# Kernel tuning notes

Measured on AMD Instinct MI355X. Metric: run time of the kernel, lower is better.

The kernel has to match this reference:

```python
import jax, jax.numpy as jnp
import numpy as np

B, C, H, W = 256, 3, 224, 224
NP, PS = 14, 16          # patches per row, patch size
D, NH, NB = 192, 4, 3    # hidden_d, num_heads (Block default), n_blocks
OUT = 1000
T = NP * NP + 1          # tokens incl. class token


def _lin(x, w, b):
    # torch nn.Linear: y = x @ W^T + b, W is [out, in]
    return x @ w.T + b


def setup_inputs() -> dict:
    key = jax.random.key(0)
    ks = jax.random.split(key, 22)
    n = lambda k, shp: jax.random.normal(k, shp, dtype=jnp.float32) * 0.02
    return {
        "x": jax.random.normal(ks[0], (B, C, H, W), dtype=jnp.float32),
        "lm_w": n(ks[1], (D, C * PS * PS)), "lm_b": n(ks[2], (D,)),
        "cls_tok": jax.random.uniform(ks[3], (1, D), dtype=jnp.float32),  # torch.rand
        "pos_emb": n(ks[4], (T, D)),
        # per-block params stacked on leading dim NB
        "q_w": n(ks[5], (NB, D, D)), "q_b": n(ks[6], (NB, D)),
        "k_w": n(ks[7], (NB, D, D)), "k_b": n(ks[8], (NB, D)),
        "v_w": n(ks[9], (NB, D, D)), "v_b": n(ks[10], (NB, D)),
        "in_w": n(ks[11], (NB, 3 * D, D)), "in_b": n(ks[12], (NB, 3 * D)),
        "out_w": n(ks[13], (NB, D, D)), "out_b": n(ks[14], (NB, D)),
        "up_w": n(ks[15], (NB, 4 * D, D)), "up_b": n(ks[16], (NB, 4 * D)),
        "down_w": n(ks[17], (NB, D, 4 * D)), "down_b": n(ks[18], (NB, D)),
        "head_w": n(ks[19], (OUT, D)), "head_b": n(ks[20], (OUT,)),
    }


def reference(x, lm_w, lm_b, cls_tok, pos_emb, q_w, q_b, k_w, k_b, v_w, v_b,
              in_w, in_b, out_w, out_b, up_w, up_b, down_w, down_b, head_w, head_b):
    N = x.shape[0]
    # vectorized patchify: [N,C,H,W] -> [N, NP*NP, C*PS*PS] (flatten order C,ps,ps matches torch)
    patches = x.reshape(N, C, NP, PS, NP, PS).transpose(0, 2, 4, 1, 3, 5).reshape(N, NP * NP, C * PS * PS)
    tok = _lin(patches, lm_w, lm_b)
    tok = jnp.concatenate([jnp.broadcast_to(cls_tok[None], (N, 1, D)), tok], axis=1) + pos_emb[None]
    dh = D // NH
    scale = 1.0 / np.sqrt(dh).astype(np.float32)
    for i in range(NB):
        # Block's own q/k/v projections
        q = _lin(tok, q_w[i], q_b[i])
        k = _lin(tok, k_w[i], k_b[i])
        v = _lin(tok, v_w[i], v_b[i])
        # nn.MultiheadAttention internal in_proj (applied on top of q/k/v)
        wq, wk, wv = jnp.split(in_w[i], 3, axis=0)
        bq, bk, bv = jnp.split(in_b[i], 3, axis=0)
        qh = _lin(q, wq, bq).reshape(N, T, NH, dh).transpose(0, 2, 1, 3)
        kh = _lin(k, wk, bk).reshape(N, T, NH, dh).transpose(0, 2, 1, 3)
        vh = _lin(v, wv, bv).reshape(N, T, NH, dh).transpose(0, 2, 1, 3)
        scores = jnp.einsum('bhqd,bhkd->bhqk', qh, kh) * scale
        attn = jax.nn.softmax(scores, axis=-1)
        o = jnp.einsum('bhqk,bhkd->bhqd', attn, vh).transpose(0, 2, 1, 3).reshape(N, T, D)
        o = _lin(o, out_w[i], out_b[i])  # MHA out_proj
        tok = tok + o                     # residual around attention only
        tok = _lin(jax.nn.relu(_lin(tok, up_w[i], up_b[i])), down_w[i], down_b[i])  # MLP, no residual
    cls = tok[:, 0, :]
    return _lin(cls, head_w, head_b)
```

## Files before the change

### kernel.cpp

```cpp
#include <hip/hip_runtime.h>

typedef unsigned short u16;
typedef __bf16 bf16x8 __attribute__((ext_vector_type(8)));
typedef float  f32x4  __attribute__((ext_vector_type(4)));
typedef u16    u16x8  __attribute__((ext_vector_type(8)));

#define BATCH 256
#define TT    197
#define TP    256
#define DD    192
#define DHP   64
#define MTOK  (BATCH*TT)
#define MPAT  (BATCH*196)

constexpr size_t BIG_E  = 1024ull*256*256;
constexpr size_t TOK_E  = (size_t)MTOK*DD;
constexpr size_t QKV_E  = 1024ull*TP*DHP;

__device__ __forceinline__ float b2f(u16 h){ union{unsigned u; float f;} x; x.u=(unsigned)h<<16; return x.f; }
__device__ __forceinline__ u16 f2b(float f){ union{float f; unsigned u;} x{f}; unsigned r = x.u + 0x7fffu + ((x.u>>16)&1u); return (u16)(r>>16); }
__device__ __forceinline__ bf16x8 as_bf(u16x8 v){ return __builtin_bit_cast(bf16x8, v); }

__device__ __forceinline__ void gload_lds16(const void* g, void* l) {
  __builtin_amdgcn_global_load_lds((__attribute__((address_space(1))) void*)(size_t)g,
                                   (__attribute__((address_space(3))) void*)l, 16, 0, 0);
}

enum { M_F32=0, M_BF16=1, M_QKV=2, M_PATCH=4 };

template<int MODE, bool RELU, bool RES, bool BIAS>
__global__ __launch_bounds__(256)
void gemm4w(const u16* __restrict__ A, const u16* __restrict__ W,
            const float* __restrict__ bias, const u16* __restrict__ res,
            void* __restrict__ Cout, const float* __restrict__ aux,
            int K, int lda, int ldc, int Nreal,
            long bA, long bW, long bC)
{
  __shared__ __align__(16) u16 As[2][256*32];
  __shared__ __align__(16) u16 Ws[2][64*32];
  const int tid  = threadIdx.x;
  const int wv   = tid >> 6;
  const int lane = tid & 63;

  const int nN  = gridDim.x, nM = gridDim.y;
  const int nwg = nN * nM;
  const int fid = blockIdx.x + nN * blockIdx.y;
  const int xcd = fid & 7, loc = fid >> 3;
  const int q8  = nwg >> 3, r8 = nwg & 7;
  const int tile = (xcd < r8 ? xcd * (q8 + 1) : r8 * (q8 + 1) + (xcd - r8) * q8) + loc;
  const int m0 = (tile / nN) * 256;
  const int n0 = (tile % nN) * 64;

  const int bz = blockIdx.z;
  const u16* Ab = A + (size_t)bz * (size_t)bA;
  const u16* Wb = W + (size_t)bz * (size_t)bW;

  const int lrow = lane & 15, quad = lane >> 4;
  const int srow = lane >> 2, sseg = lane & 3;
  const int wsw  = (srow >> 1) & 3;
  const int rsw  = (lrow >> 1) & 3;

  f32x4 acc[4][4];
  #pragma unroll
  for (int i=0;i<4;i++)
    #pragma unroll
    for (int j=0;j<4;j++) { f32x4 z = {0.f,0.f,0.f,0.f}; acc[i][j] = z; }

  auto stage = [&](int bufi, int k0) {
    #pragma unroll
    for (int i=0;i<4;i++) {
      const u16* ga = Ab + (size_t)(m0 + i*64 + wv*16 + srow)*lda + (k0 + (sseg^wsw)*8);
      gload_lds16(ga, &As[bufi][(i*64 + wv*16)*32]);
    }
    const u16* gw = Wb + (size_t)(n0 + wv*16 + srow)*K + (k0 + (sseg^wsw)*8);
    gload_lds16(gw, &Ws[bufi][(wv*16)*32]);
  };

  const int nt = K >> 5;
  stage(0, 0);
  int cur = 0;
  for (int t = 0; t < nt; ++t) {
    if (t + 1 < nt) {
      stage(cur ^ 1, (t + 1) << 5);
      asm volatile("s_waitcnt vmcnt(5)" ::: "memory");
    } else {
      asm volatile("s_waitcnt vmcnt(0)" ::: "memory");
    }
    asm volatile("s_barrier" ::: "memory");

    bf16x8 af[4], wf[4];
    #pragma unroll
    for (int i=0;i<4;i++) {
      af[i] = *(const bf16x8*)&As[cur][(wv*64 + i*16 + lrow)*32 + (quad^rsw)*8];
      wf[i] = *(const bf16x8*)&Ws[cur][(i*16 + lrow)*32 + (quad^rsw)*8];
    }
    #pragma unroll
    for (int mi=0;mi<4;mi++)
      #pragma unroll
      for (int ni=0;ni<4;ni++)
        acc[mi][ni] = __builtin_amdgcn_mfma_f32_16x16x32_bf16(af[mi], wf[ni], acc[mi][ni], 0,0,0);

    asm volatile("s_waitcnt lgkmcnt(0)" ::: "memory");
    asm volatile("s_barrier" ::: "memory");
    cur ^= 1;
  }

  #pragma unroll
  for (int mi=0;mi<4;mi++) {
    #pragma unroll
    for (int ni=0;ni<4;ni++) {
      #pragma unroll
      for (int r=0;r<4;r++) {
        int row = m0 + wv*64 + mi*16 + quad*4 + r;
        int col = n0 + ni*16 + lrow;
        float v = acc[mi][ni][r];
        if constexpr (MODE == M_F32) {
          if (col < Nreal) {
            if constexpr (BIAS) v += bias[col];
            ((float*)Cout)[(size_t)row*ldc + col] = v;
          }
        } else if constexpr (MODE == M_BF16) {
          if constexpr (BIAS) v += bias[col];
          if constexpr (RES)  v += b2f(res[(size_t)row*ldc + col]);
          if constexpr (RELU) v = v > 0.f ? v : 0.f;
          ((u16*)Cout)[(size_t)bz*(size_t)bC + (size_t)row*ldc + col] = f2b(v);
        } else if constexpr (MODE == M_QKV) {
          v += bias[col];
          int sel = col / 192, rem = col % 192;
          int h = rem / 48, d = rem % 48;
          int b = row / 197, t = row % 197;
          ((u16*)Cout)[(size_t)sel*QKV_E + ((size_t)(b*4 + h)*TP + t)*DHP + d] = f2b(v);
        } else if constexpr (MODE == M_PATCH) {
          int b = row / 196, p = row % 196;
          v += bias[col] + aux[(size_t)(1 + p)*DD + col];
          ((u16*)Cout)[((size_t)(b*197) + 1 + p)*DD + col] = f2b(v);
        }
      }
    }
  }
}

#define KSTR 72
#define VSTR 216
#define PSTR 72
#define TKR  208

__global__ __launch_bounds__(256,1)
void flash_k(const u16* __restrict__ Qg, const u16* __restrict__ Kg,
             const u16* __restrict__ Vg, u16* __restrict__ Og)
{
  __shared__ __align__(16) u16 Ks[TKR*KSTR];
  __shared__ __align__(16) u16 Vs[49*VSTR];
  __shared__ __align__(16) u16 Ps[4*16*PSTR];
  const int bh = blockIdx.x;
  const int b = bh >> 2, h = bh & 3;
  const int tid = threadIdx.x, wv = tid >> 6, lane = tid & 63;
  const int lrow = lane & 15, quad = lane >> 4;
  const size_t base = (size_t)bh * TP * DHP;
  const float scale = 0.14433756729740643f;

  bf16x8 qf[4][2];
  #pragma unroll
  for (int rg=0; rg<4; rg++)
    #pragma unroll
    for (int ka=0; ka<2; ka++)
      qf[rg][ka] = as_bf(*(const u16x8*)(Qg + base + (size_t)(wv*64+rg*16+lrow)*DHP + ka*32 + quad*8));

  for (int it=0; it<5; it++) {
    int slot = it*256 + tid;
    if (slot < 1248) {
      int t = slot/6, sg = slot - t*6;
      u16x8 v = *(const u16x8*)(Kg + base + (size_t)t*DHP + sg*8);
      *(u16x8*)&Ks[t*KSTR + sg*8] = v;
    }
  }
  {
    u16x8 z = {0,0,0,0,0,0,0,0};
    for (int it=0; it<2; it++) {
      int slot = it*256 + tid;
      if (slot < 416) { int t = slot>>1, sg = 6 + (slot&1);
        *(u16x8*)&Ks[t*KSTR + sg*8] = z; }
    }
  }
  for (int it=0; it<5; it++) {
    int slot = it*256 + tid;
    if (slot < 1248) {
      int sg = slot/208, t = slot - sg*208;
      u16x8 v = *(const u16x8*)(Vg + base + (size_t)t*DHP + sg*8);
      #pragma unroll
      for (int j=0;j<8;j++) Vs[(sg*8+j)*VSTR + t] = v[j];
    }
  }
  __syncthreads();

  f32x4 o[4][3];
  float m_i[4][4], l_i[4][4];
  #pragma unroll
  for (int rg=0;rg<4;rg++) {
    #pragma unroll
    for (int dg=0;dg<3;dg++) { f32x4 z = {0.f,0.f,0.f,0.f}; o[rg][dg] = z; }
    #pragma unroll
    for (int r=0;r<4;r++) { m_i[rg][r] = -1e30f; l_i[rg][r] = 0.f; }
  }
  u16* Pw = &Ps[wv*16*PSTR];

  #pragma unroll
  for (int c=0; c<4; c++) {
    const int NC = (c<3) ? 4 : 1;
    f32x4 s[4][4];
    #pragma unroll
    for (int rg=0;rg<4;rg++)
      #pragma unroll
      for (int cg=0;cg<4;cg++) if (cg < NC) { f32x4 z = {0.f,0.f,0.f,0.f}; s[rg][cg] = z; }

    #pragma unroll
    for (int cg=0;cg<4;cg++) if (cg < NC) {
      #pragma unroll
      for (int ka=0; ka<2; ka++) {
        bf16x8 kf = as_bf(*(const u16x8*)&Ks[(c*64+cg*16+lrow)*KSTR + ka*32 + quad*8]);
        #pragma unroll
        for (int rg=0;rg<4;rg++)
          s[rg][cg] = __builtin_amdgcn_mfma_f32_16x16x32_bf16(qf[rg][ka], kf, s[rg][cg], 0,0,0);
      }
    }

    #pragma unroll
    for (int rg=0;rg<4;rg++) {
      if (c == 3) {
        #pragma unroll
        for (int r=0;r<4;r++) s[rg][0][r] = (lrow >= 5) ? -1e30f : s[rg][0][r];
      }
      float mnew[4], al[4];
      #pragma unroll
      for (int r=0;r<4;r++) {
        float mc = s[rg][0][r];
        #pragma unroll
        for (int cg=1;cg<4;cg++) if (cg < NC) mc = fmaxf(mc, s[rg][cg][r]);
        #pragma unroll
        for (int sh=1; sh<16; sh<<=1) mc = fmaxf(mc, __shfl_xor(mc, sh, 64));
        float mo = m_i[rg][r];
        float mn = fmaxf(mo, mc);
        mnew[r] = mn;
        al[r] = __expf((mo - mn)*scale);
      }
      #pragma unroll
      for (int r=0;r<4;r++) {
        float acc = 0.f;
        #pragma unroll
        for (int cg=0;cg<4;cg++) if (cg < NC) {
          float p = __expf((s[rg][cg][r] - mnew[r])*scale);
          s[rg][cg][r] = p;
          acc += p;
        }
        #pragma unroll
        for (int sh=1; sh<16; sh<<=1) acc += __shfl_xor(acc, sh, 64);
        l_i[rg][r] = l_i[rg][r]*al[r] + acc;
        m_i[rg][r] = mnew[r];
      }
      #pragma unroll
      for (int dg=0;dg<3;dg++)
        #pragma unroll
        for (int r=0;r<4;r++) o[rg][dg][r] *= al[r];

      #pragma unroll
      for (int cg=0;cg<4;cg++) if (cg < NC) {
        #pragma unroll
        for (int r=0;r<4;r++)
          Pw[(quad*4+r)*PSTR + cg*16 + lrow] = f2b(s[rg][cg][r]);
      }
      if (c == 3) {
        #pragma unroll
        for (int r=0;r<4;r++) Pw[(quad*4+r)*PSTR + 16 + lrow] = 0;
      }
      __builtin_amdgcn_s_waitcnt(0xC07F);

      const int NK = (c<3) ? 2 : 1;
      #pragma unroll
      for (int ka=0; ka<2; ka++) if (ka < NK) {
        bf16x8 pf = as_bf(*(const u16x8*)&Pw[lrow*PSTR + ka*32 + quad*8]);
        #pragma unroll
        for (int dg=0;dg<3;dg++) {
          bf16x8 vf = as_bf(*(const u16x8*)&Vs[(dg*16+lrow)*VSTR + c*64 + ka*32 + quad*8]);
          o[rg][dg] = __builtin_amdgcn_mfma_f32_16x16x32_bf16(pf, vf, o[rg][dg], 0,0,0);
        }
      }
      __builtin_amdgcn_s_waitcnt(0xC07F);
    }
  }

  #pragma unroll
  for (int rg=0;rg<4;rg++) {
    #pragma unroll
    for (int r=0;r<4;r++) {
      int t = wv*64 + rg*16 + quad*4 + r;
      if (t < 197) {
        float inv = 1.0f / l_i[rg][r];
        u16* dst = Og + ((size_t)(b*197) + t)*DD + h*48;
        #pragma unroll
        for (int dg=0;dg<3;dg++) dst[dg*16 + lrow] = f2b(o[rg][dg][r]*inv);
      }
    }
  }
}

__global__ void cvt5_k(const float* __restrict__ a, const float* __restrict__ b,
                       const float* __restrict__ c, const float* __restrict__ d,
                       const float* __restrict__ e,
                       u16* __restrict__ oa, u16* __restrict__ ob, u16* __restrict__ oc,
                       u16* __restrict__ od, u16* __restrict__ oe) {
  int i = blockIdx.x*256 + threadIdx.x;
  if (i < 147456) { oa[i] = f2b(a[i]); return; } i -= 147456;
  if (i < 110592) { ob[i] = f2b(b[i]); return; } i -= 110592;
  if (i < 442368) { oc[i] = f2b(c[i]); return; } i -= 442368;
  if (i < 442368) { od[i] = f2b(d[i]); return; } i -= 442368;
  if (i < 196608) { oe[i] = (i < 192000) ? f2b(e[i]) : (u16)0; }
}

__global__ void im2col_k(const float* __restrict__ x, u16* __restrict__ P) {
  int id = blockIdx.x*256 + threadIdx.x;
  int w8 = id % 28; int r = id / 28;
  int h  = r % 224; r /= 224;
  int c  = r % 3;   int b = r / 3;
  const float* src = x + (((size_t)(b*3 + c)*224 + h)*224 + w8*8);
  float4 a  = *(const float4*)src;
  float4 bb = *(const float4*)(src + 4);
  int pr = h >> 4, i = h & 15, pc = (w8*8) >> 4, j0 = (w8*8) & 15;
  u16* dst = P + ((size_t)(b*196) + pr*14 + pc)*768 + (c*256 + i*16 + j0);
  u16x8 o;
  o[0]=f2b(a.x); o[1]=f2b(a.y); o[2]=f2b(a.z); o[3]=f2b(a.w);
  o[4]=f2b(bb.x); o[5]=f2b(bb.y); o[6]=f2b(bb.z); o[7]=f2b(bb.w);
  *(u16x8*)dst = o;
}

__global__ void cls_k(const float* __restrict__ cls_tok, const float* __restrict__ pos, u16* __restrict__ tok) {
  int b = blockIdx.x, d = threadIdx.x;
  tok[((size_t)b*197)*DD + d] = f2b(cls_tok[d] + pos[d]);
}

__global__ void fusew_k(const float* __restrict__ in_w, const float* __restrict__ q_w,
                        const float* __restrict__ k_w, const float* __restrict__ v_w,
                        u16* __restrict__ weff) {
  int i = blockIdx.x, p = blockIdx.y, n = blockIdx.z;
  int k = threadIdx.x;
  const float* wrow = in_w + ((size_t)i*576 + p*192 + n)*192;
  const float* Bm = (p==0 ? q_w : (p==1 ? k_w : v_w)) + (size_t)i*192*192;
  float acc = 0.f;
  for (int m=0;m<192;m++) acc += wrow[m] * Bm[m*192 + k];
  weff[((size_t)i*576 + p*192 + n)*192 + k] = f2b(acc);
}

__global__ void fuseb_k(const float* __restrict__ in_w, const float* __restrict__ q_b,
                        const float* __restrict__ k_b, const float* __restrict__ v_b,
                        const float* __restrict__ in_b, float* __restrict__ effb) {
  int i = blockIdx.x, n = threadIdx.x;
  int p = n / 192;
  const float* bb = (p==0 ? q_b : (p==1 ? k_b : v_b)) + i*192;
  const float* wrow = in_w + ((size_t)i*576 + n)*192;
  float acc = in_b[i*576 + n];
  for (int m=0;m<192;m++) acc += wrow[m]*bb[m];
  effb[i*576 + n] = acc;
}

extern "C" void kernel_launch(void* const* d_in, const int* in_sizes, int n_in,
                              void* d_out, int out_size, void* d_ws, size_t ws_size,
                              hipStream_t stream) {
  const float* x      = (const float*)d_in[0];
  const float* lm_w   = (const float*)d_in[1];
  const float* lm_b   = (const float*)d_in[2];
  const float* cls_t  = (const float*)d_in[3];
  const float* pos    = (const float*)d_in[4];
  const float* q_w    = (const float*)d_in[5];
  const float* q_b    = (const float*)d_in[6];
  const float* k_w    = (const float*)d_in[7];
  const float* k_b    = (const float*)d_in[8];
  const float* v_w    = (const float*)d_in[9];
  const float* v_b    = (const float*)d_in[10];
  const float* in_w   = (const float*)d_in[11];
  const float* in_b   = (const float*)d_in[12];
  const float* out_w  = (const float*)d_in[13];
  const float* out_b  = (const float*)d_in[14];
  const float* up_w   = (const float*)d_in[15];
  const float* up_b   = (const float*)d_in[16];
  const float* dn_w   = (const float*)d_in[17];
  const float* dn_b   = (const float*)d_in[18];
  const float* head_w = (const float*)d_in[19];
  const float* head_b = (const float*)d_in[20];

  char* ws = (char*)d_ws;
  size_t off = 0;
  auto alloc = [&](size_t elems, size_t esz) {
    void* p = ws + off; off += ((elems*esz + 255)/256)*256; return p;
  };
  u16*  big  = (u16*)alloc(BIG_E, 2);
  u16*  tok  = (u16*)alloc(TOK_E, 2);
  u16*  qq   = (u16*)alloc(QKV_E*3, 2);
  u16*  obuf = (u16*)alloc(TOK_E, 2);
  u16*  lmw  = (u16*)alloc(147456, 2);
  u16*  outw = (u16*)alloc(110592, 2);
  u16*  upw  = (u16*)alloc(442368, 2);
  u16*  dnw  = (u16*)alloc(442368, 2);
  u16*  hdw  = (u16*)alloc(196608, 2);
  u16*  weff = (u16*)alloc(331776, 2);
  float* effb = (float*)alloc(1728, 4);
  (void)ws_size; (void)in_sizes; (void)n_in; (void)out_size;

  u16* kbuf = qq + QKV_E;
  u16* vbuf = qq + 2*QKV_E;

  cvt5_k<<<(1339392+255)/256,256,0,stream>>>(lm_w, out_w, up_w, dn_w, head_w,
                                             lmw, outw, upw, dnw, hdw);
  fusew_k<<<dim3(3,3,192),192,0,stream>>>(in_w, q_w, k_w, v_w, weff);
  fuseb_k<<<3,576,0,stream>>>(in_w, q_b, k_b, v_b, in_b, effb);

  im2col_k<<<18816,256,0,stream>>>(x, big);
  gemm4w<M_PATCH,false,false,true><<<dim3(3,MPAT/256,1),256,0,stream>>>(
      big, lmw, lm_b, nullptr, tok, pos, 768, 768, DD, DD, 0,0,0);
  cls_k<<<BATCH,DD,0,stream>>>(cls_t, pos, tok);

  for (int i=0;i<3;i++) {
    gemm4w<M_QKV,false,false,true><<<dim3(9,MTOK/256,1),256,0,stream>>>(
        tok, weff + (size_t)i*576*192, effb + i*576, nullptr, qq, nullptr,
        192, 192, 0, 576, 0,0,0);
    flash_k<<<1024,256,0,stream>>>(qq, kbuf, vbuf, obuf);
    gemm4w<M_BF16,false,true,true><<<dim3(3,MTOK/256,1),256,0,stream>>>(
        obuf, outw + (size_t)i*36864, out_b + i*192, tok, tok, nullptr,
        192, 192, DD, DD, 0,0,0);
    gemm4w<M_BF16,true,false,true><<<dim3(12,MTOK/256,1),256,0,stream>>>(
        tok, upw + (size_t)i*147456, up_b + i*768, nullptr, big, nullptr,
        192, 192, 768, 768, 0,0,0);
    gemm4w<M_BF16,false,false,true><<<dim3(3,MTOK/256,1),256,0,stream>>>(
        big, dnw + (size_t)i*147456, dn_b + i*192, nullptr, tok, nullptr,
        768, 768, DD, DD, 0,0,0);
  }
  gemm4w<M_F32,false,false,true><<<dim3(16,1,1),256,0,stream>>>(
      tok, hdw, head_b, nullptr, d_out, nullptr,
      192, 197*192, 1000, 1000, 0,0,0);
}
```

Measured before the change: 981.5 us.

## Halve GEMM M-tile, triple-buffer LDS, and software-pipeline flash P·V

The GEMM kernel's M tile shrinks from 256 to 128 rows, giving twice as many workgroups. It moves from double to triple buffering, prefetching two K-steps ahead with a single barrier per iteration instead of two. The flash attention kernel double-buffers the P scratch per wave so the P·V MFMAs for the previous row group overlap the softmax of the current one, with the last P·V drained after the loop. Risks include the single-barrier triple-buffer race safety and more LDS traffic per FLOP from smaller tiles. MTOK=50432 is divisible by 128, so the grid changes stay consistent.

```diff
diff --git a/kernel.cpp b/kernel.cpp
--- a/kernel.cpp
+++ b/kernel.cpp
@@ -36,8 +36,8 @@
             int K, int lda, int ldc, int Nreal,
             long bA, long bW, long bC)
 {
-  __shared__ __align__(16) u16 As[2][256*32];
-  __shared__ __align__(16) u16 Ws[2][64*32];
+  __shared__ __align__(16) u16 As[3][128*32];
+  __shared__ __align__(16) u16 Ws[3][64*32];
   const int tid  = threadIdx.x;
   const int wv   = tid >> 6;
   const int lane = tid & 63;
@@ -48,7 +48,7 @@
   const int xcd = fid & 7, loc = fid >> 3;
   const int q8  = nwg >> 3, r8 = nwg & 7;
   const int tile = (xcd < r8 ? xcd * (q8 + 1) : r8 * (q8 + 1) + (xcd - r8) * q8) + loc;
-  const int m0 = (tile / nN) * 256;
+  const int m0 = (tile / nN) * 128;
   const int n0 = (tile % nN) * 64;
 
   const int bz = blockIdx.z;
@@ -60,15 +60,15 @@
   const int wsw  = (srow >> 1) & 3;
   const int rsw  = (lrow >> 1) & 3;
 
-  f32x4 acc[4][4];
-  #pragma unroll
-  for (int i=0;i<4;i++)
+  f32x4 acc[2][4];
+  #pragma unroll
+  for (int i=0;i<2;i++)
     #pragma unroll
     for (int j=0;j<4;j++) { f32x4 z = {0.f,0.f,0.f,0.f}; acc[i][j] = z; }
 
   auto stage = [&](int bufi, int k0) {
     #pragma unroll
-    for (int i=0;i<4;i++) {
+    for (int i=0;i<2;i++) {
       const u16* ga = Ab + (size_t)(m0 + i*64 + wv*16 + srow)*lda + (k0 + (sseg^wsw)*8);
       gload_lds16(ga, &As[bufi][(i*64 + wv*16)*32]);
     }
@@ -78,40 +78,38 @@
 
   const int nt = K >> 5;
   stage(0, 0);
-  int cur = 0;
+  stage(1, 32);
   for (int t = 0; t < nt; ++t) {
     if (t + 1 < nt) {
-      stage(cur ^ 1, (t + 1) << 5);
-      asm volatile("s_waitcnt vmcnt(5)" ::: "memory");
+      asm volatile("s_waitcnt vmcnt(3)" ::: "memory");
     } else {
       asm volatile("s_waitcnt vmcnt(0)" ::: "memory");
     }
     asm volatile("s_barrier" ::: "memory");
-
-    bf16x8 af[4], wf[4];
-    #pragma unroll
-    for (int i=0;i<4;i++) {
-      af[i] = *(const bf16x8*)&As[cur][(wv*64 + i*16 + lrow)*32 + (quad^rsw)*8];
+    if (t + 2 < nt) stage((t + 2) % 3, (t + 2) << 5);
+
+    const int cur = t % 3;
+    bf16x8 af[2], wf[4];
+    #pragma unroll
+    for (int i=0;i<2;i++)
+      af[i] = *(const bf16x8*)&As[cur][(wv*32 + i*16 + lrow)*32 + (quad^rsw)*8];
+    #pragma unroll
+    for (int i=0;i<4;i++)
       wf[i] = *(const bf16x8*)&Ws[cur][(i*16 + lrow)*32 + (quad^rsw)*8];
-    }
-    #pragma unroll
-    for (int mi=0;mi<4;mi++)
+    #pragma unroll
+    for (int mi=0;mi<2;mi++)
       #pragma unroll
       for (int ni=0;ni<4;ni++)
         acc[mi][ni] = __builtin_amdgcn_mfma_f32_16x16x32_bf16(af[mi], wf[ni], acc[mi][ni], 0,0,0);
-
-    asm volatile("s_waitcnt lgkmcnt(0)" ::: "memory");
-    asm volatile("s_barrier" ::: "memory");
-    cur ^= 1;
-  }
-
-  #pragma unroll
-  for (int mi=0;mi<4;mi++) {
+  }
+
+  #pragma unroll
+  for (int mi=0;mi<2;mi++) {
     #pragma unroll
     for (int ni=0;ni<4;ni++) {
       #pragma unroll
       for (int r=0;r<4;r++) {
-        int row = m0 + wv*64 + mi*16 + quad*4 + r;
+        int row = m0 + wv*32 + mi*16 + quad*4 + r;
         int col = n0 + ni*16 + lrow;
         float v = acc[mi][ni][r];
         if constexpr (MODE == M_F32) {
@@ -151,7 +149,7 @@
 {
   __shared__ __align__(16) u16 Ks[TKR*KSTR];
   __shared__ __align__(16) u16 Vs[49*VSTR];
-  __shared__ __align__(16) u16 Ps[4*16*PSTR];
+  __shared__ __align__(16) u16 Ps[8*16*PSTR];
   const int bh = blockIdx.x;
   const int b = bh >> 2, h = bh & 3;
   const int tid = threadIdx.x, wv = tid >> 6, lane = tid & 63;
@@ -202,7 +200,8 @@
     #pragma unroll
     for (int r=0;r<4;r++) { m_i[rg][r] = -1e30f; l_i[rg][r] = 0.f; }
   }
-  u16* Pw = &Ps[wv*16*PSTR];
+  u16* PwA = &Ps[(wv*2 + 0)*16*PSTR];
+  u16* PwB = &Ps[(wv*2 + 1)*16*PSTR];
 
   #pragma unroll
   for (int c=0; c<4; c++) {
@@ -226,6 +225,7 @@
 
     #pragma unroll
     for (int rg=0;rg<4;rg++) {
+      const int it  = c*4 + rg;
       if (c == 3) {
         #pragma unroll
         for (int r=0;r<4;r++) s[rg][0][r] = (lrow >= 5) ? -1e30f : s[rg][0][r];
@@ -257,34 +257,48 @@
         l_i[rg][r] = l_i[rg][r]*al[r] + acc;
         m_i[rg][r] = mnew[r];
       }
+
+      if (it > 0) {
+        const int pit = it - 1, ppc = pit >> 2, pprg = pit & 3;
+        const int NKp = (ppc < 3) ? 2 : 1;
+        const u16* Pr = (pit & 1) ? PwB : PwA;
+        __builtin_amdgcn_s_waitcnt(0xC07F);
+        #pragma unroll
+        for (int ka=0; ka<2; ka++) if (ka < NKp) {
+          bf16x8 pf = as_bf(*(const u16x8*)&Pr[lrow*PSTR + ka*32 + quad*8]);
+          #pragma unroll
+          for (int dg=0;dg<3;dg++) {
+            bf16x8 vf = as_bf(*(const u16x8*)&Vs[(dg*16+lrow)*VSTR + ppc*64 + ka*32 + quad*8]);
+            o[pprg][dg] = __builtin_amdgcn_mfma_f32_16x16x32_bf16(pf, vf, o[pprg][dg], 0,0,0);
+          }
+        }
+      }
+
       #pragma unroll
       for (int dg=0;dg<3;dg++)
         #pragma unroll
         for (int r=0;r<4;r++) o[rg][dg][r] *= al[r];
 
+      u16* Pd = (it & 1) ? PwB : PwA;
       #pragma unroll
       for (int cg=0;cg<4;cg++) if (cg < NC) {
         #pragma unroll
         for (int r=0;r<4;r++)
-          Pw[(quad*4+r)*PSTR + cg*16 + lrow] = f2b(s[rg][cg][r]);
+          Pd[(quad*4+r)*PSTR + cg*16 + lrow] = f2b(s[rg][cg][r]);
       }
       if (c == 3) {
         #pragma unroll
-        for (int r=0;r<4;r++) Pw[(quad*4+r)*PSTR + 16 + lrow] = 0;
-      }
-      __builtin_amdgcn_s_waitcnt(0xC07F);
-
-      const int NK = (c<3) ? 2 : 1;
-      #pragma unroll
-      for (int ka=0; ka<2; ka++) if (ka < NK) {
-        bf16x8 pf = as_bf(*(const u16x8*)&Pw[lrow*PSTR + ka*32 + quad*8]);
-        #pragma unroll
-        for (int dg=0;dg<3;dg++) {
-          bf16x8 vf = as_bf(*(const u16x8*)&Vs[(dg*16+lrow)*VSTR + c*64 + ka*32 + quad*8]);
-          o[rg][dg] = __builtin_amdgcn_mfma_f32_16x16x32_bf16(pf, vf, o[rg][dg], 0,0,0);
-        }
-      }
-      __builtin_amdgcn_s_waitcnt(0xC07F);
+        for (int r=0;r<4;r++) Pd[(quad*4+r)*PSTR + 16 + lrow] = 0;
+      }
+    }
+  }
+  {
+    __builtin_amdgcn_s_waitcnt(0xC07F);
+    bf16x8 pf = as_bf(*(const u16x8*)&PwB[lrow*PSTR + quad*8]);
+    #pragma unroll
+    for (int dg=0;dg<3;dg++) {
+      bf16x8 vf = as_bf(*(const u16x8*)&Vs[(dg*16+lrow)*VSTR + 3*64 + quad*8]);
+      o[3][dg] = __builtin_amdgcn_mfma_f32_16x16x32_bf16(pf, vf, o[3][dg], 0,0,0);
     }
   }
 
@@ -413,26 +427,26 @@
   fuseb_k<<<3,576,0,stream>>>(in_w, q_b, k_b, v_b, in_b, effb);
 
   im2col_k<<<18816,256,0,stream>>>(x, big);
-  gemm4w<M_PATCH,false,false,true><<<dim3(3,MPAT/256,1),256,0,stream>>>(
+  gemm4w<M_PATCH,false,false,true><<<dim3(3,MPAT/128,1),256,0,stream>>>(
       big, lmw, lm_b, nullptr, tok, pos, 768, 768, DD, DD, 0,0,0);
   cls_k<<<BATCH,DD,0,stream>>>(cls_t, pos, tok);
 
   for (int i=0;i<3;i++) {
-    gemm4w<M_QKV,false,false,true><<<dim3(9,MTOK/256,1),256,0,stream>>>(
+    gemm4w<M_QKV,false,false,true><<<dim3(9,MTOK/128,1),256,0,stream>>>(
         tok, weff + (size_t)i*576*192, effb + i*576, nullptr, qq, nullptr,
         192, 192, 0, 576, 0,0,0);
     flash_k<<<1024,256,0,stream>>>(qq, kbuf, vbuf, obuf);
-    gemm4w<M_BF16,false,true,true><<<dim3(3,MTOK/256,1),256,0,stream>>>(
+    gemm4w<M_BF16,false,true,true><<<dim3(3,MTOK/128,1),256,0,stream>>>(
         obuf, outw + (size_t)i*36864, out_b + i*192, tok, tok, nullptr,
         192, 192, DD, DD, 0,0,0);
-    gemm4w<M_BF16,true,false,true><<<dim3(12,MTOK/256,1),256,0,stream>>>(
+    gemm4w<M_BF16,true,false,true><<<dim3(12,MTOK/128,1),256,0,stream>>>(
         tok, upw + (size_t)i*147456, up_b + i*768, nullptr, big, nullptr,
         192, 192, 768, 768, 0,0,0);
-    gemm4w<M_BF16,false,false,true><<<dim3(3,MTOK/256,1),256,0,stream>>>(
+    gemm4w<M_BF16,false,false,true><<<dim3(3,MTOK/128,1),256,0,stream>>>(
         big, dnw + (size_t)i*147456, dn_b + i*192, nullptr, tok, nullptr,
         768, 768, DD, DD, 0,0,0);
   }
-  gemm4w<M_F32,false,false,true><<<dim3(16,1,1),256,0,stream>>>(
+  gemm4w<M_F32,false,false,true><<<dim3(16,2,1),256,0,stream>>>(
       tok, hdw, head_b, nullptr, d_out, nullptr,
       192, 197*192, 1000, 1000, 0,0,0);
 }
```

New measurement: 973.8 us. No clear change (-0.8%).
